# Kernel optimization log

Measured on AMD Instinct MI355X. Metric: run time of the kernel, lower is better.

Reference implementation:

```python
import jax, jax.numpy as jnp
import numpy as np

D_MODEL, N_HEADS, D_C, D_COMP, D_ROPE = 2048, 16, 512, 768, 64
D_HEAD = D_MODEL // N_HEADS  # 128
B, S = 2, 2048
ROPE_THETA = 10000.0


def _rope_cos_sin(seq_len, dim):
    # frequencies for pairwise complex rotation, dim = per-head rope dim (even)
    inv_freq = 1.0 / (ROPE_THETA ** (jnp.arange(0, dim, 2, dtype=jnp.float32) / dim))
    t = jnp.arange(seq_len, dtype=jnp.float32)
    ang = t[:, None] * inv_freq[None, :]  # [S, dim/2]
    return jnp.cos(ang), jnp.sin(ang)


def _apply_rope(x, cos, sin):
    # x: [B, S, H, dr]; rotate consecutive pairs (view_as_complex semantics)
    x1, x2 = x[..., 0::2], x[..., 1::2]
    c = cos[None, :, None, :]
    s = sin[None, :, None, :]
    y1 = x1 * c - x2 * s
    y2 = x1 * s + x2 * c
    return jnp.stack([y1, y2], axis=-1).reshape(x.shape)


def setup_inputs() -> dict:
    key = jax.random.key(0)
    ks = jax.random.split(key, 9)
    sc = 0.02
    return {
        "x": jax.random.normal(ks[0], (B, S, D_MODEL), jnp.float32),
        "Wd": jax.random.normal(ks[1], (D_MODEL, D_C), jnp.float32) * sc,
        "bd": jnp.zeros((D_C,), jnp.float32),
        "Wu": jax.random.normal(ks[2], (D_C, N_HEADS * D_HEAD), jnp.float32) * sc,
        "bu": jnp.zeros((N_HEADS * D_HEAD,), jnp.float32),
        "Wqd": jax.random.normal(ks[3], (D_MODEL, D_COMP), jnp.float32) * sc,
        "bqd": jnp.zeros((D_COMP,), jnp.float32),
        "Wqu": jax.random.normal(ks[4], (D_COMP, N_HEADS * D_HEAD), jnp.float32) * sc,
        "bqu": jnp.zeros((N_HEADS * D_HEAD,), jnp.float32),
        "Wqr": jax.random.normal(ks[5], (D_COMP, N_HEADS * D_ROPE), jnp.float32) * sc,
        "bqr": jnp.zeros((N_HEADS * D_ROPE,), jnp.float32),
        "Wkr": jax.random.normal(ks[6], (D_MODEL, N_HEADS * D_ROPE), jnp.float32) * sc,
        "bkr": jnp.zeros((N_HEADS * D_ROPE,), jnp.float32),
        "Wo": jax.random.normal(ks[7], (N_HEADS * D_HEAD, D_MODEL), jnp.float32) * sc,
        "bo": jnp.zeros((D_MODEL,), jnp.float32),
    }


def reference(x, Wd, bd, Wu, bu, Wqd, bqd, Wqu, bqu, Wqr, bqr, Wkr, bkr, Wo, bo):
    b, s, _ = x.shape
    # low-rank KV compression
    kv_c = x @ Wd + bd                                   # [B,S,d_c]
    kv_up = (kv_c @ Wu + bu).reshape(b, s, N_HEADS, D_HEAD)  # shared K-content / V
    # low-rank Q compression
    q_cmp = x @ Wqd + bqd                                # [B,S,d_comp]
    q_c = (q_cmp @ Wqu + bqu).reshape(b, s, N_HEADS, D_HEAD)
    # decoupled RoPE branches
    cos, sin = _rope_cos_sin(s, D_ROPE)
    q_r = _apply_rope((q_cmp @ Wqr + bqr).reshape(b, s, N_HEADS, D_ROPE), cos, sin)
    k_r = _apply_rope((x @ Wkr + bkr).reshape(b, s, N_HEADS, D_ROPE), cos, sin)
    q = jnp.concatenate([q_c, q_r], axis=-1)             # [B,S,H,dh+dr]
    k = jnp.concatenate([kv_up, k_r], axis=-1)           # [B,S,H,dh+dr]
    scale = 1.0 / np.sqrt(D_HEAD).astype(np.float32)
    scores = jnp.einsum('bqhd,bkhd->bhqk', q, k) * scale  # [B,H,S,S]
    probs = jax.nn.softmax(scores, axis=-1)
    out = jnp.einsum('bhqk,bkhd->bqhd', probs, kv_up)    # v == kv_up (as in source)
    out = out.reshape(b, s, N_HEADS * D_HEAD)
    return out @ Wo + bo
```

## Files before the change

### kernel.cpp

```cpp
#include <hip/hip_runtime.h>
#include <cmath>

typedef __bf16 bf16;
typedef __bf16 bf16x8 __attribute__((ext_vector_type(8)));
typedef __bf16 bf16x4 __attribute__((ext_vector_type(4)));
typedef float f32x4 __attribute__((ext_vector_type(4)));
typedef int i32x4 __attribute__((ext_vector_type(4)));

#define S_LEN 2048
#define QK_LD 3072

__device__ __forceinline__ void async_copy16(const bf16* g, bf16* l) {
    __builtin_amdgcn_global_load_lds(
        (const __attribute__((address_space(1))) void*)g,
        (__attribute__((address_space(3))) void*)l, 16, 0, 0);
}

__global__ __launch_bounds__(256) void cast_f32_bf16(const float* __restrict__ in,
                                                     bf16* __restrict__ out) {
    size_t i = ((size_t)blockIdx.x * 256 + threadIdx.x) * 8;
    float4 a = *(const float4*)(in + i);
    float4 b = *(const float4*)(in + i + 4);
    bf16x8 v;
    v[0] = (bf16)a.x; v[1] = (bf16)a.y; v[2] = (bf16)a.z; v[3] = (bf16)a.w;
    v[4] = (bf16)b.x; v[5] = (bf16)b.y; v[6] = (bf16)b.z; v[7] = (bf16)b.w;
    *(bf16x8*)(out + i) = v;
}

struct TSeg { const float* src; bf16* dst; int K, N, blk0; };
struct TArgs { TSeg s[7]; };

__global__ __launch_bounds__(256) void transpose_all(TArgs a) {
    __shared__ float tile[64][68];
    int b = blockIdx.x, si = 0;
#pragma unroll
    for (int i = 1; i < 7; ++i) if (b >= a.s[i].blk0) si = i;
    TSeg sg = a.s[si];
    int local = b - sg.blk0;
    int kTiles = sg.K >> 6;
    int kt = local % kTiles, nt = local / kTiles;
    int k0 = kt * 64, n0 = nt * 64;
    int K = sg.K, N = sg.N;
    int t = threadIdx.x;
#pragma unroll
    for (int i = 0; i < 4; ++i) {
        int c = t + i * 256;
        int r = c >> 4, off = (c & 15) * 4;
        float4 v = *(const float4*)(sg.src + (size_t)(k0 + r) * N + n0 + off);
        tile[r][off] = v.x; tile[r][off + 1] = v.y;
        tile[r][off + 2] = v.z; tile[r][off + 3] = v.w;
    }
    __syncthreads();
#pragma unroll
    for (int i = 0; i < 2; ++i) {
        int c = t + i * 256;
        int nr = c >> 3, koff = (c & 7) * 8;
        bf16x8 v;
#pragma unroll
        for (int j = 0; j < 8; ++j) v[j] = (bf16)tile[koff + j][nr];
        *(bf16x8*)(sg.dst + (size_t)(n0 + nr) * K + k0 + koff) = v;
    }
}

__global__ __launch_bounds__(256) void setup_small(const float* __restrict__ bd,
                                                   const float* __restrict__ bqd,
                                                   const float* __restrict__ bkr,
                                                   const float* __restrict__ bqu,
                                                   const float* __restrict__ bqr,
                                                   float* __restrict__ bcat,
                                                   float2* __restrict__ tab) {
    if (blockIdx.x < 21) {
        int i = blockIdx.x * 256 + threadIdx.x;
        if (i < 512) bcat[i] = bd[i];
        else if (i < 1280) bcat[i] = bqd[i - 512];
        else if (i < 2304) bcat[i] = bkr[i - 1280];
        else if (i < 4352) bcat[i] = bqu[i - 2304];
        else if (i < 5376) bcat[i] = bqr[i - 4352];
    } else {
        int id = (blockIdx.x - 21) * 256 + threadIdx.x;
        int s = id >> 5, i = id & 31;
        float f = expf(-0.2878231366242557f * (float)i);
        float ang = (float)s * f;
        tab[id] = make_float2(cosf(ang), sinf(ang));
    }
}

__device__ __forceinline__ void gemm_core(const bf16* __restrict__ A, int lda,
                                          const bf16* __restrict__ Bt,
                                          const float* __restrict__ bias,
                                          void* __restrict__ out0,
                                          void* __restrict__ out1,
                                          int Ndim, int Kdim, int mode,
                                          const float2* __restrict__ tab,
                                          int bn, int bm, bf16* As, bf16* Bs) {
    int t = threadIdx.x;
    int w = t >> 6, lane = t & 63;
    int wm = (w >> 1) * 64, wn = (w & 1) * 64;
    int l15 = lane & 15, q4 = lane >> 4;
    f32x4 acc[4][4] = {};

    int lrow = lane >> 2;
    int lcol = (lane & 3) * 8;
    int c0 = w * 2, c1 = w * 2 + 1;
    const bf16* aS0 = A  + (size_t)(bm * 128 + c0 * 16 + lrow) * lda + lcol;
    const bf16* aS1 = A  + (size_t)(bm * 128 + c1 * 16 + lrow) * lda + lcol;
    const bf16* bS0 = Bt + (size_t)(bn * 128 + c0 * 16 + lrow) * Kdim + lcol;
    const bf16* bS1 = Bt + (size_t)(bn * 128 + c1 * 16 + lrow) * Kdim + lcol;
    bf16* aD0 = &As[c0 * 512]; bf16* aD1 = &As[c1 * 512];
    bf16* bD0 = &Bs[c0 * 512]; bf16* bD1 = &Bs[c1 * 512];

    for (int kt = 0; kt < Kdim; kt += 32) {
        async_copy16(aS0 + kt, aD0);
        async_copy16(aS1 + kt, aD1);
        async_copy16(bS0 + kt, bD0);
        async_copy16(bS1 + kt, bD1);
        __syncthreads();
        bf16x8 af[4], bfr[4];
#pragma unroll
        for (int mb = 0; mb < 4; ++mb)
            af[mb] = *(const bf16x8*)&As[(wm + mb * 16 + l15) * 32 + q4 * 8];
#pragma unroll
        for (int nb = 0; nb < 4; ++nb)
            bfr[nb] = *(const bf16x8*)&Bs[(wn + nb * 16 + l15) * 32 + q4 * 8];
#pragma unroll
        for (int mb = 0; mb < 4; ++mb)
#pragma unroll
            for (int nb = 0; nb < 4; ++nb)
                acc[mb][nb] = __builtin_amdgcn_mfma_f32_16x16x32_bf16(
                    af[mb], bfr[nb], acc[mb][nb], 0, 0, 0);
        __syncthreads();
    }

#pragma unroll
    for (int mb = 0; mb < 4; ++mb) {
        int row = bm * 128 + wm + mb * 16 + q4 * 4;
#pragma unroll
        for (int nb = 0; nb < 4; ++nb) {
            int col = bn * 128 + wn + nb * 16 + l15;
            float bv = bias[col];
            if (mode == 1) {
#pragma unroll
                for (int r = 0; r < 4; ++r)
                    ((float*)out0)[(size_t)(row + r) * Ndim + col] = acc[mb][nb][r] + bv;
            } else if (mode == 4) {
                if (col < 1280) {
#pragma unroll
                    for (int r = 0; r < 4; ++r)
                        ((bf16*)out0)[(size_t)(row + r) * 2304 + col] =
                            (bf16)(acc[mb][nb][r] + bv);
                } else {
                    int rel = col - 1280;
                    int hh = rel >> 6, idx = rel & 63, ii = idx >> 1, odd = idx & 1;
#pragma unroll
                    for (int r = 0; r < 4; ++r) {
                        float vv = acc[mb][nb][r] + bv;
                        float pp = __shfl_xor(vv, 1, 64);
                        float2 cs = tab[((row + r) & 2047) * 32 + ii];
                        float o = vv * cs.x + (odd ? pp * cs.y : -pp * cs.y);
                        ((bf16*)out1)[(size_t)(row + r) * QK_LD + hh * 192 + 128 + idx] =
                            (bf16)o;
                    }
                }
            } else if (mode == 5) {
                if (col < 2048) {
                    int hh = col >> 7, dd = col & 127;
#pragma unroll
                    for (int r = 0; r < 4; ++r)
                        ((bf16*)out0)[(size_t)(row + r) * QK_LD + hh * 192 + dd] =
                            (bf16)(acc[mb][nb][r] + bv);
                } else {
                    int rel = col - 2048;
                    int hh = rel >> 6, idx = rel & 63, ii = idx >> 1, odd = idx & 1;
#pragma unroll
                    for (int r = 0; r < 4; ++r) {
                        float vv = acc[mb][nb][r] + bv;
                        float pp = __shfl_xor(vv, 1, 64);
                        float2 cs = tab[((row + r) & 2047) * 32 + ii];
                        float o = vv * cs.x + (odd ? pp * cs.y : -pp * cs.y);
                        ((bf16*)out0)[(size_t)(row + r) * QK_LD + hh * 192 + 128 + idx] =
                            (bf16)o;
                    }
                }
            } else {
                int hh = col >> 7, dd = col & 127;
                bf16x4 pack;
#pragma unroll
                for (int r = 0; r < 4; ++r) {
                    float vv = acc[mb][nb][r] + bv;
                    ((bf16*)out0)[(size_t)(row + r) * QK_LD + hh * 192 + dd] = (bf16)vv;
                    pack[r] = (bf16)vv;
                }
                int bidx = row >> 11, srow = row & 2047;
                *(bf16x4*)((bf16*)out1 +
                           ((size_t)(bidx * 16 + hh) * 128 + dd) * S_LEN + srow) = pack;
            }
        }
    }
}

__global__ __launch_bounds__(256) void gemm_bt(const bf16* __restrict__ A, int lda,
                                               const bf16* __restrict__ Bt,
                                               const float* __restrict__ bias,
                                               void* __restrict__ out0,
                                               void* __restrict__ out1,
                                               int Ndim, int Kdim, int mode,
                                               const float2* __restrict__ tab) {
    __shared__ bf16 As[128 * 32];
    __shared__ bf16 Bs[128 * 32];
    gemm_core(A, lda, Bt, bias, out0, out1, Ndim, Kdim, mode, tab,
              blockIdx.x, blockIdx.y, As, Bs);
}

__global__ __launch_bounds__(256) void gemm_up(const bf16* __restrict__ xproj,
                                               const bf16* __restrict__ WuT,
                                               const float* __restrict__ bu,
                                               void* __restrict__ kbuf,
                                               void* __restrict__ vt,
                                               const bf16* __restrict__ W2T,
                                               const float* __restrict__ bq,
                                               void* __restrict__ qbuf,
                                               const float2* __restrict__ tab) {
    __shared__ bf16 As[128 * 32];
    __shared__ bf16 Bs[128 * 32];
    int bn = blockIdx.x;
    if (bn < 16)
        gemm_core(xproj, 2304, WuT, bu, kbuf, vt, 2048, 512, 6, tab,
                  bn, blockIdx.y, As, Bs);
    else
        gemm_core(xproj + 512, 2304, W2T, bq, qbuf, nullptr, 3072, 768, 5, tab,
                  bn - 16, blockIdx.y, As, Bs);
}

__global__ __launch_bounds__(256, 2) void attn(const bf16* __restrict__ qbuf,
                                               const bf16* __restrict__ kbuf,
                                               const bf16* __restrict__ vt,
                                               bf16* __restrict__ attnout) {
    __shared__ bf16 Ks[64 * 200];
    __shared__ bf16 Vs[128 * 72];
    __shared__ bf16 Ps[128 * 72];
    int bh = blockIdx.x;
    int qt = blockIdx.y;
    int b = bh >> 4, h = bh & 15;
    int t = threadIdx.x, w = t >> 6, lane = t & 63;
    int l15 = lane & 15, q4 = lane >> 4;
    const float scale = 0.08838834764831845f;

    bf16x8 qf[2][6];
    {
        size_t base = (size_t)(b * S_LEN + qt * 128 + w * 32) * QK_LD + h * 192;
#pragma unroll
        for (int mb = 0; mb < 2; ++mb)
#pragma unroll
            for (int c = 0; c < 6; ++c)
                qf[mb][c] = *(const bf16x8*)(qbuf + base +
                            (size_t)(mb * 16 + l15) * QK_LD + c * 32 + q4 * 8);
    }

    f32x4 oacc[2][8] = {};
    float denom[2] = {0.f, 0.f};
    const bf16* kb_base = kbuf + (size_t)b * S_LEN * QK_LD + h * 192;
    const bf16* vt_base = vt + (size_t)bh * 128 * S_LEN;

    int kr_[6], ko_[6], vd_[4], vo_[4];
#pragma unroll
    for (int i = 0; i < 6; ++i) { int c = t + (i << 8); kr_[i] = c / 24; ko_[i] = (c % 24) * 8; }
#pragma unroll
    for (int i = 0; i < 4; ++i) { int c = t + (i << 8); vd_[i] = c >> 3; vo_[i] = (c & 7) * 8; }

    i32x4 kreg[6], vreg[4];
#pragma unroll
    for (int i = 0; i < 6; ++i)
        kreg[i] = *(const i32x4*)(kb_base + (size_t)kr_[i] * QK_LD + ko_[i]);
#pragma unroll
    for (int i = 0; i < 4; ++i)
        vreg[i] = *(const i32x4*)(vt_base + (size_t)vd_[i] * S_LEN + vo_[i]);

    for (int kt = 0; kt < 32; ++kt) {
        __syncthreads();
#pragma unroll
        for (int i = 0; i < 6; ++i) *(i32x4*)&Ks[kr_[i] * 200 + ko_[i]] = kreg[i];
#pragma unroll
        for (int i = 0; i < 4; ++i) *(i32x4*)&Vs[vd_[i] * 72 + vo_[i]] = vreg[i];
        __syncthreads();
        if (kt < 31) {
#pragma unroll
            for (int i = 0; i < 6; ++i)
                kreg[i] = *(const i32x4*)(kb_base +
                          (size_t)((kt + 1) * 64 + kr_[i]) * QK_LD + ko_[i]);
#pragma unroll
            for (int i = 0; i < 4; ++i)
                vreg[i] = *(const i32x4*)(vt_base +
                          (size_t)vd_[i] * S_LEN + (kt + 1) * 64 + vo_[i]);
        }

        f32x4 sacc[2][4] = {};
#pragma unroll
        for (int c = 0; c < 6; ++c) {
#pragma unroll
            for (int nk = 0; nk < 4; ++nk) {
                bf16x8 kb = *(const bf16x8*)&Ks[(nk * 16 + l15) * 200 + c * 32 + q4 * 8];
#pragma unroll
                for (int mb = 0; mb < 2; ++mb)
                    sacc[mb][nk] = __builtin_amdgcn_mfma_f32_16x16x32_bf16(
                        kb, qf[mb][c], sacc[mb][nk], 0, 0, 0);
            }
        }

#pragma unroll
        for (int mb = 0; mb < 2; ++mb)
#pragma unroll
            for (int nk = 0; nk < 4; ++nk) {
                bf16x4 pk;
#pragma unroll
                for (int r = 0; r < 4; ++r) {
                    float p = __expf(fminf(sacc[mb][nk][r] * scale, 50.0f));
                    denom[mb] += p;
                    pk[r] = (bf16)p;
                }
                *(bf16x4*)&Ps[(w * 32 + mb * 16 + l15) * 72 + nk * 16 + q4 * 4] = pk;
            }

#pragma unroll
        for (int kc = 0; kc < 2; ++kc) {
            bf16x8 pa[2];
#pragma unroll
            for (int mb = 0; mb < 2; ++mb)
                pa[mb] = *(const bf16x8*)&Ps[(w * 32 + mb * 16 + l15) * 72 +
                                             kc * 32 + q4 * 8];
#pragma unroll
            for (int nb = 0; nb < 8; ++nb) {
                bf16x8 vb = *(const bf16x8*)&Vs[(nb * 16 + l15) * 72 + kc * 32 + q4 * 8];
#pragma unroll
                for (int mb = 0; mb < 2; ++mb)
                    oacc[mb][nb] = __builtin_amdgcn_mfma_f32_16x16x32_bf16(
                        pa[mb], vb, oacc[mb][nb], 0, 0, 0);
            }
        }
    }

#pragma unroll
    for (int mb = 0; mb < 2; ++mb) {
        denom[mb] += __shfl_xor(denom[mb], 16, 64);
        denom[mb] += __shfl_xor(denom[mb], 32, 64);
    }

#pragma unroll
    for (int mb = 0; mb < 2; ++mb)
#pragma unroll
        for (int r = 0; r < 4; ++r) {
            float dv = __shfl(denom[mb], q4 * 4 + r, 64);
            float inv = 1.0f / dv;
            int row = qt * 128 + w * 32 + mb * 16 + q4 * 4 + r;
#pragma unroll
            for (int nb = 0; nb < 8; ++nb) {
                int col = h * 128 + nb * 16 + l15;
                attnout[(size_t)(b * S_LEN + row) * 2048 + col] =
                    (bf16)(oacc[mb][nb][r] * inv);
            }
        }
}

extern "C" void kernel_launch(void* const* d_in, const int* in_sizes, int n_in,
                              void* d_out, int out_size, void* d_ws, size_t ws_size,
                              hipStream_t stream) {
    const float* x   = (const float*)d_in[0];
    const float* Wd  = (const float*)d_in[1];
    const float* bd  = (const float*)d_in[2];
    const float* Wu  = (const float*)d_in[3];
    const float* bu  = (const float*)d_in[4];
    const float* Wqd = (const float*)d_in[5];
    const float* bqd = (const float*)d_in[6];
    const float* Wqu = (const float*)d_in[7];
    const float* bqu = (const float*)d_in[8];
    const float* Wqr = (const float*)d_in[9];
    const float* bqr = (const float*)d_in[10];
    const float* Wkr = (const float*)d_in[11];
    const float* bkr = (const float*)d_in[12];
    const float* Wo  = (const float*)d_in[13];
    const float* bo  = (const float*)d_in[14];
    float* out = (float*)d_out;

    char* p = (char*)d_ws;
    auto alloc = [&](size_t n) { char* r = p; p += (n + 255) & ~(size_t)255; return r; };
    bf16* xb    = (bf16*)alloc((size_t)4096 * 2048 * 2);
    bf16* W1T   = (bf16*)alloc((size_t)2304 * 2048 * 2);
    bf16* W2T   = (bf16*)alloc((size_t)3072 * 768 * 2);
    bf16* WuT   = (bf16*)alloc((size_t)2048 * 512 * 2);
    bf16* WoT   = (bf16*)alloc((size_t)2048 * 2048 * 2);
    bf16* xproj = (bf16*)alloc((size_t)4096 * 2304 * 2);
    bf16* qbuf  = (bf16*)alloc((size_t)4096 * 3072 * 2);
    bf16* kbuf  = (bf16*)alloc((size_t)4096 * 3072 * 2);
    bf16* vt    = (bf16*)alloc((size_t)32 * 128 * 2048 * 2);
    bf16* aout  = (bf16*)alloc((size_t)4096 * 2048 * 2);
    float* bcat = (float*)alloc((size_t)5376 * 4);
    float2* tab = (float2*)alloc((size_t)65536 * 8);

    cast_f32_bf16<<<dim3(4096), dim3(256), 0, stream>>>(x, xb);

    TArgs ta;
    ta.s[0] = {Wd,  W1T,                       2048, 512,  0};
    ta.s[1] = {Wqd, W1T + (size_t)512 * 2048,  2048, 768,  256};
    ta.s[2] = {Wkr, W1T + (size_t)1280 * 2048, 2048, 1024, 640};
    ta.s[3] = {Wqu, W2T,                       768,  2048, 1152};
    ta.s[4] = {Wqr, W2T + (size_t)2048 * 768,  768,  1024, 1536};
    ta.s[5] = {Wu,  WuT,                       512,  2048, 1728};
    ta.s[6] = {Wo,  WoT,                       2048, 2048, 1984};
    transpose_all<<<dim3(3008), dim3(256), 0, stream>>>(ta);
    setup_small<<<dim3(277), dim3(256), 0, stream>>>(bd, bqd, bkr, bqu, bqr, bcat, tab);

    gemm_bt<<<dim3(18, 32), dim3(256), 0, stream>>>(xb, 2048, W1T, bcat,
                                                    xproj, kbuf, 2304, 2048, 4, tab);
    gemm_up<<<dim3(40, 32), dim3(256), 0, stream>>>(xproj, WuT, bu, kbuf, vt,
                                                    W2T, bcat + 2304, qbuf, tab);

    attn<<<dim3(32, 16), dim3(256), 0, stream>>>(qbuf, kbuf, vt, aout);

    gemm_bt<<<dim3(16, 32), dim3(256), 0, stream>>>(aout, 2048, WoT, bo,
                                                    out, nullptr, 2048, 2048, 1, tab);
}
```

Before: 434.8 us.

## Split attention waves 2x2 over query/key tiles and prescale Q for exp2

New measurement: 545.7 us. +25.5%, slower.

```diff
diff --git a/kernel.cpp b/kernel.cpp
--- a/kernel.cpp
+++ b/kernel.cpp
@@ -9,6 +9,7 @@
 
 #define S_LEN 2048
 #define QK_LD 3072
+#define Q_PRESCALE 0.12751742566146944f
 
 __device__ __forceinline__ void async_copy16(const bf16* g, bf16* l) {
     __builtin_amdgcn_global_load_lds(
@@ -167,7 +168,7 @@
 #pragma unroll
                     for (int r = 0; r < 4; ++r)
                         ((bf16*)out0)[(size_t)(row + r) * QK_LD + hh * 192 + dd] =
-                            (bf16)(acc[mb][nb][r] + bv);
+                            (bf16)((acc[mb][nb][r] + bv) * Q_PRESCALE);
                 } else {
                     int rel = col - 2048;
                     int hh = rel >> 6, idx = rel & 63, ii = idx >> 1, odd = idx & 1;
@@ -178,7 +179,7 @@
                         float2 cs = tab[((row + r) & 2047) * 32 + ii];
                         float o = vv * cs.x + (odd ? pp * cs.y : -pp * cs.y);
                         ((bf16*)out0)[(size_t)(row + r) * QK_LD + hh * 192 + 128 + idx] =
-                            (bf16)o;
+                            (bf16)(o * Q_PRESCALE);
                     }
                 }
             } else {
@@ -238,26 +239,27 @@
     __shared__ bf16 Ks[64 * 200];
     __shared__ bf16 Vs[128 * 72];
     __shared__ bf16 Ps[128 * 72];
+    __shared__ float denomLds[2][128];
     int bh = blockIdx.x;
     int qt = blockIdx.y;
     int b = bh >> 4, h = bh & 15;
     int t = threadIdx.x, w = t >> 6, lane = t & 63;
+    int wq = w >> 1, wk = w & 1;
     int l15 = lane & 15, q4 = lane >> 4;
-    const float scale = 0.08838834764831845f;
-
-    bf16x8 qf[2][6];
+
+    bf16x8 qf[4][6];
     {
-        size_t base = (size_t)(b * S_LEN + qt * 128 + w * 32) * QK_LD + h * 192;
-#pragma unroll
-        for (int mb = 0; mb < 2; ++mb)
+        size_t base = (size_t)(b * S_LEN + qt * 128 + wq * 64) * QK_LD + h * 192;
+#pragma unroll
+        for (int mb = 0; mb < 4; ++mb)
 #pragma unroll
             for (int c = 0; c < 6; ++c)
                 qf[mb][c] = *(const bf16x8*)(qbuf + base +
                             (size_t)(mb * 16 + l15) * QK_LD + c * 32 + q4 * 8);
     }
 
-    f32x4 oacc[2][8] = {};
-    float denom[2] = {0.f, 0.f};
+    f32x4 oacc[4][4] = {};
+    float denom[4] = {};
     const bf16* kb_base = kbuf + (size_t)b * S_LEN * QK_LD + h * 192;
     const bf16* vt_base = vt + (size_t)bh * 128 * S_LEN;
 
@@ -293,69 +295,76 @@
                           (size_t)vd_[i] * S_LEN + (kt + 1) * 64 + vo_[i]);
         }
 
-        f32x4 sacc[2][4] = {};
-#pragma unroll
-        for (int c = 0; c < 6; ++c) {
-#pragma unroll
-            for (int nk = 0; nk < 4; ++nk) {
-                bf16x8 kb = *(const bf16x8*)&Ks[(nk * 16 + l15) * 200 + c * 32 + q4 * 8];
-#pragma unroll
-                for (int mb = 0; mb < 2; ++mb)
-                    sacc[mb][nk] = __builtin_amdgcn_mfma_f32_16x16x32_bf16(
-                        kb, qf[mb][c], sacc[mb][nk], 0, 0, 0);
+#pragma unroll
+        for (int nk = 0; nk < 2; ++nk) {
+            f32x4 sacc[4] = {};
+#pragma unroll
+            for (int c = 0; c < 6; ++c) {
+                bf16x8 kb = *(const bf16x8*)&Ks[(wk * 32 + nk * 16 + l15) * 200 +
+                                                c * 32 + q4 * 8];
+#pragma unroll
+                for (int mb = 0; mb < 4; ++mb)
+                    sacc[mb] = __builtin_amdgcn_mfma_f32_16x16x32_bf16(
+                        kb, qf[mb][c], sacc[mb], 0, 0, 0);
             }
-        }
-
-#pragma unroll
-        for (int mb = 0; mb < 2; ++mb)
-#pragma unroll
-            for (int nk = 0; nk < 4; ++nk) {
+#pragma unroll
+            for (int mb = 0; mb < 4; ++mb) {
                 bf16x4 pk;
 #pragma unroll
                 for (int r = 0; r < 4; ++r) {
-                    float p = __expf(fminf(sacc[mb][nk][r] * scale, 50.0f));
+                    float p = exp2f(fminf(sacc[mb][r], 80.0f));
                     denom[mb] += p;
                     pk[r] = (bf16)p;
                 }
-                *(bf16x4*)&Ps[(w * 32 + mb * 16 + l15) * 72 + nk * 16 + q4 * 4] = pk;
-            }
-
-#pragma unroll
-        for (int kc = 0; kc < 2; ++kc) {
-            bf16x8 pa[2];
-#pragma unroll
-            for (int mb = 0; mb < 2; ++mb)
-                pa[mb] = *(const bf16x8*)&Ps[(w * 32 + mb * 16 + l15) * 72 +
-                                             kc * 32 + q4 * 8];
-#pragma unroll
-            for (int nb = 0; nb < 8; ++nb) {
-                bf16x8 vb = *(const bf16x8*)&Vs[(nb * 16 + l15) * 72 + kc * 32 + q4 * 8];
-#pragma unroll
-                for (int mb = 0; mb < 2; ++mb)
-                    oacc[mb][nb] = __builtin_amdgcn_mfma_f32_16x16x32_bf16(
-                        pa[mb], vb, oacc[mb][nb], 0, 0, 0);
+                *(bf16x4*)&Ps[(wq * 64 + mb * 16 + l15) * 72 +
+                              wk * 32 + nk * 16 + q4 * 4] = pk;
             }
         }
-    }
-
-#pragma unroll
-    for (int mb = 0; mb < 2; ++mb) {
+        __syncthreads();
+
+#pragma unroll
+        for (int kc = 0; kc < 2; ++kc) {
+            bf16x8 pa[4];
+#pragma unroll
+            for (int mb = 0; mb < 4; ++mb)
+                pa[mb] = *(const bf16x8*)&Ps[(wq * 64 + mb * 16 + l15) * 72 +
+                                             kc * 32 + q4 * 8];
+#pragma unroll
+            for (int nd = 0; nd < 4; ++nd) {
+                bf16x8 vb = *(const bf16x8*)&Vs[(wk * 64 + nd * 16 + l15) * 72 +
+                                                kc * 32 + q4 * 8];
+#pragma unroll
+                for (int mb = 0; mb < 4; ++mb)
+                    oacc[mb][nd] = __builtin_amdgcn_mfma_f32_16x16x32_bf16(
+                        pa[mb], vb, oacc[mb][nd], 0, 0, 0);
+            }
+        }
+    }
+
+#pragma unroll
+    for (int mb = 0; mb < 4; ++mb) {
         denom[mb] += __shfl_xor(denom[mb], 16, 64);
         denom[mb] += __shfl_xor(denom[mb], 32, 64);
     }
-
-#pragma unroll
-    for (int mb = 0; mb < 2; ++mb)
+    if (q4 == 0) {
+#pragma unroll
+        for (int mb = 0; mb < 4; ++mb)
+            denomLds[wk][wq * 64 + mb * 16 + l15] = denom[mb];
+    }
+    __syncthreads();
+
+#pragma unroll
+    for (int mb = 0; mb < 4; ++mb)
 #pragma unroll
         for (int r = 0; r < 4; ++r) {
-            float dv = __shfl(denom[mb], q4 * 4 + r, 64);
-            float inv = 1.0f / dv;
-            int row = qt * 128 + w * 32 + mb * 16 + q4 * 4 + r;
-#pragma unroll
-            for (int nb = 0; nb < 8; ++nb) {
-                int col = h * 128 + nb * 16 + l15;
+            int rl = wq * 64 + mb * 16 + q4 * 4 + r;
+            float inv = 1.0f / (denomLds[0][rl] + denomLds[1][rl]);
+            int row = qt * 128 + rl;
+#pragma unroll
+            for (int nd = 0; nd < 4; ++nd) {
+                int col = h * 128 + wk * 64 + nd * 16 + l15;
                 attnout[(size_t)(b * S_LEN + row) * 2048 + col] =
-                    (bf16)(oacc[mb][nb][r] * inv);
+                    (bf16)(oacc[mb][nd][r] * inv);
             }
         }
 }
```
